# Performance work log

Hardware: AMD Instinct MI355X
Metric: run time of the kernel (lower is better)

## Reference

```python
import jax, jax.numpy as jnp
import numpy as np

NUM_HEADS = 16
HIDDEN = 64  # per-head dim


def setup_inputs() -> dict:
    key = jax.random.key(0)
    ks = jax.random.split(key, 7)
    B, Nq, S, D = 2, 2048, 2048, 1024
    return {
        "queries": jax.random.normal(ks[0], (B, Nq, D), jnp.float32),
        "keys": jax.random.normal(ks[1], (B, S, D), jnp.float32),
        "values": jax.random.normal(ks[2], (B, S, D), jnp.float32),
        "Wq": jax.random.normal(ks[3], (D, NUM_HEADS * HIDDEN), jnp.float32) * 0.02,
        "Wk": jax.random.normal(ks[4], (D, NUM_HEADS * HIDDEN), jnp.float32) * 0.02,
        "Wv": jax.random.normal(ks[5], (D, NUM_HEADS * HIDDEN), jnp.float32) * 0.02,
        "Wo": jax.random.normal(ks[6], (NUM_HEADS * HIDDEN, 1024), jnp.float32) * 0.02,
    }


def reference(queries, keys, values, Wq, Wk, Wv, Wo):
    B, Nq, _ = queries.shape
    S = keys.shape[1]
    H, dh = NUM_HEADS, HIDDEN
    # projections, split heads: [B, len, H, dh] -> [B, H, len, dh]
    Q = (queries @ Wq).reshape(B, Nq, H, dh).transpose(0, 2, 1, 3)
    K = (keys @ Wk).reshape(B, S, H, dh).transpose(0, 2, 1, 3)
    V = (values @ Wv).reshape(B, S, H, dh).transpose(0, 2, 1, 3)
    scores = jnp.einsum("bhqd,bhkd->bhqk", Q, K) / jnp.sqrt(jnp.float32(dh))
    # NOTE: faithful to original -- softmax over ALL keys, THEN multiply by
    # strictly-lower-triangular mask (triangular * (1 - diagonal)); no renorm.
    P = jax.nn.softmax(scores, axis=-1)
    mask = jnp.tril(jnp.ones((Nq, S), jnp.float32), -1)  # strict lower triangle
    Sout = jnp.einsum("bhqk,bhkd->bhqd", P * mask, V)
    merged = Sout.transpose(0, 2, 1, 3).reshape(B, Nq, H * dh)
    return merged @ Wo
```

## Files before the change

kernel.cpp:

```cpp
#include <hip/hip_runtime.h>
#include <hip/hip_bf16.h>
#include <stdint.h>


typedef __bf16 bf16x8 __attribute__((ext_vector_type(8)));
typedef float f32x4 __attribute__((ext_vector_type(4)));

typedef const __attribute__((address_space(1))) void* gas_t;
typedef __attribute__((address_space(3))) void* las_t;

__device__ __forceinline__ unsigned short f2bf(float f) {
    unsigned int u = __float_as_uint(f);
    return (unsigned short)((u + 0x7FFFu + ((u >> 16) & 1u)) >> 16);
}

__global__ __launch_bounds__(256) void cast_qkv(
    const float* __restrict__ q, const float* __restrict__ k, const float* __restrict__ v,
    unsigned short* __restrict__ oq, unsigned short* __restrict__ ok, unsigned short* __restrict__ ov)
{
    const float* src = (blockIdx.z == 0) ? q : (blockIdx.z == 1) ? k : v;
    unsigned short* dst = (blockIdx.z == 0) ? oq : (blockIdx.z == 1) ? ok : ov;
    unsigned int i = blockIdx.x * 256u + threadIdx.x;
    float4 f = reinterpret_cast<const float4*>(src)[i];
    ushort4 o;
    o.x = f2bf(f.x); o.y = f2bf(f.y); o.z = f2bf(f.z); o.w = f2bf(f.w);
    reinterpret_cast<ushort4*>(dst)[i] = o;
}

__global__ __launch_bounds__(256) void transpose_w(
    const float* __restrict__ w0, const float* __restrict__ w1,
    const float* __restrict__ w2, const float* __restrict__ w3,
    unsigned short* __restrict__ t0, unsigned short* __restrict__ t1,
    unsigned short* __restrict__ t2, unsigned short* __restrict__ t3)
{
    const float* W = (blockIdx.z == 0) ? w0 : (blockIdx.z == 1) ? w1 : (blockIdx.z == 2) ? w2 : w3;
    unsigned short* T = (blockIdx.z == 0) ? t0 : (blockIdx.z == 1) ? t1 : (blockIdx.z == 2) ? t2 : t3;
    __shared__ float s[32][33];
    const int tx = threadIdx.x, ty = threadIdx.y;
    const int x = blockIdx.x * 32 + tx;
#pragma unroll
    for (int j = 0; j < 4; ++j)
        s[ty + 8 * j][tx] = W[(size_t)(blockIdx.y * 32 + ty + 8 * j) * 1024 + x];
    __syncthreads();
    const int xo = blockIdx.y * 32 + tx;
#pragma unroll
    for (int j = 0; j < 4; ++j)
        T[(size_t)(blockIdx.x * 32 + ty + 8 * j) * 1024 + xo] = f2bf(s[tx][ty + 8 * j]);
}

__global__ __launch_bounds__(256) void transpose_v(
    const unsigned short* __restrict__ Vp, unsigned short* __restrict__ Vt)
{
    __shared__ unsigned short s[64][68];
    const int tid = threadIdx.x;
    const int s0 = blockIdx.x * 64, h = blockIdx.y, b = blockIdx.z;
    const size_t inbase = ((size_t)(b * 2048 + s0)) * 1024 + h * 64;
#pragma unroll
    for (int r = 0; r < 4; ++r) {
        int idx = r * 256 + tid;
        int row = idx >> 4;
        int c4 = (idx & 15) * 4;
        ushort4 v = *(const ushort4*)(Vp + inbase + (size_t)row * 1024 + c4);
        *(ushort4*)&s[row][c4] = v;
    }
    __syncthreads();
    const size_t outbase = ((size_t)((b * 16 + h) * 64)) * 2048 + s0;
#pragma unroll
    for (int r = 0; r < 4; ++r) {
        int idx = r * 256 + tid;
        int drow = idx >> 4;
        int sc = (idx & 15) * 4;
        ushort4 v;
        v.x = s[sc][drow]; v.y = s[sc + 1][drow]; v.z = s[sc + 2][drow]; v.w = s[sc + 3][drow];
        *(ushort4*)(Vt + outbase + (size_t)drow * 2048 + sc) = v;
    }
}

template <int BM, int BN, int MODE>
__global__ __launch_bounds__(256) void gemm_bt(
    const unsigned short* __restrict__ A0, const unsigned short* __restrict__ A1,
    const unsigned short* __restrict__ A2,
    const unsigned short* __restrict__ B0, const unsigned short* __restrict__ B1,
    const unsigned short* __restrict__ B2,
    unsigned short* __restrict__ C0, unsigned short* __restrict__ C1,
    unsigned short* __restrict__ C2, float* __restrict__ Cf)
{
    constexpr int K = 1024;
    constexpr int WM = BM / 2, WN = BN / 2, MI = WM / 16, NI = WN / 16;
    __shared__ __align__(16) unsigned char lds[(BM + BN) * 64];
    unsigned char* lA = lds;
    unsigned char* lB = lds + BM * 64;

    const int tid = threadIdx.x;
    const int z = blockIdx.z;
    const unsigned short* A  = (MODE == 1 || z == 0) ? A0 : (z == 1) ? A1 : A2;
    const unsigned short* Bt = (MODE == 1 || z == 0) ? B0 : (z == 1) ? B1 : B2;
    const int m0 = blockIdx.y * BM, n0 = blockIdx.x * BN;
    const int w = tid >> 6, lane = tid & 63, g = lane >> 4, l15 = lane & 15;
    const int wr = w >> 1, wc = w & 1;

    f32x4 acc[MI][NI] = {};

    for (int k0 = 0; k0 < K; k0 += 32) {
#pragma unroll
        for (int r = 0; r < (BM * 64) / 4096; ++r) {
            const int o = (r * 256 + tid) * 16;
            const unsigned char* gp = (const unsigned char*)A
                + ((size_t)(m0 + (o >> 6)) * K + k0) * 2 + (o & 63);
            __builtin_amdgcn_global_load_lds((gas_t)gp,
                (las_t)(lA + (r * 256 + (tid & ~63)) * 16), 16, 0, 0);
        }
#pragma unroll
        for (int r = 0; r < (BN * 64) / 4096; ++r) {
            const int o = (r * 256 + tid) * 16;
            const unsigned char* gp = (const unsigned char*)Bt
                + ((size_t)(n0 + (o >> 6)) * K + k0) * 2 + (o & 63);
            __builtin_amdgcn_global_load_lds((gas_t)gp,
                (las_t)(lB + (r * 256 + (tid & ~63)) * 16), 16, 0, 0);
        }
        __syncthreads();

        bf16x8 a[MI], bfr[NI];
#pragma unroll
        for (int mi = 0; mi < MI; ++mi)
            a[mi] = *(const bf16x8*)(lA + (wr * WM + mi * 16 + l15) * 64 + g * 16);
#pragma unroll
        for (int ni = 0; ni < NI; ++ni)
            bfr[ni] = *(const bf16x8*)(lB + (wc * WN + ni * 16 + l15) * 64 + g * 16);
#pragma unroll
        for (int mi = 0; mi < MI; ++mi)
#pragma unroll
            for (int ni = 0; ni < NI; ++ni)
                acc[mi][ni] = __builtin_amdgcn_mfma_f32_16x16x32_bf16(a[mi], bfr[ni], acc[mi][ni], 0, 0, 0);
        __syncthreads();
    }

    if (MODE == 1) {
#pragma unroll
        for (int mi = 0; mi < MI; ++mi)
#pragma unroll
            for (int ni = 0; ni < NI; ++ni)
#pragma unroll
                for (int i = 0; i < 4; ++i) {
                    const int row = m0 + wr * WM + mi * 16 + 4 * g + i;
                    const int col = n0 + wc * WN + ni * 16 + l15;
                    Cf[(size_t)row * 1024 + col] = acc[mi][ni][i];
                }
    } else {
        unsigned short* C = (z == 0) ? C0 : (z == 1) ? C1 : C2;
#pragma unroll
        for (int mi = 0; mi < MI; ++mi)
#pragma unroll
            for (int ni = 0; ni < NI; ++ni)
#pragma unroll
                for (int i = 0; i < 4; ++i) {
                    const int row = m0 + wr * WM + mi * 16 + 4 * g + i;
                    const int col = n0 + wc * WN + ni * 16 + l15;
                    C[(size_t)row * 1024 + col] = f2bf(acc[mi][ni][i]);
                }
    }
}

__device__ __forceinline__ f32x4 qk_exp(const unsigned char* ldsbase, int rowoff,
                                        int ni, int g, int l15,
                                        bf16x8 aq0, bf16x8 aq1)
{
    const int row = rowoff + ni * 16 + l15;
    const int sw = (row & 7) << 4;
    const bf16x8 bk0 = *(const bf16x8*)(ldsbase + ((row * 128 + g * 16) ^ sw));
    const bf16x8 bk1 = *(const bf16x8*)(ldsbase + ((row * 128 + 64 + g * 16) ^ sw));
    f32x4 t = {};
    t = __builtin_amdgcn_mfma_f32_16x16x32_bf16(aq0, bk0, t, 0, 0, 0);
    t = __builtin_amdgcn_mfma_f32_16x16x32_bf16(aq1, bk1, t, 0, 0, 0);
    f32x4 r;
#pragma unroll
    for (int i = 0; i < 4; ++i) r[i] = __expf(t[i] * 0.125f);
    return r;
}

__global__ __launch_bounds__(256) void attn_kernel(
    const unsigned short* __restrict__ Qp, const unsigned short* __restrict__ Kp,
    const unsigned short* __restrict__ Vt, unsigned short* __restrict__ mrg)
{
    __shared__ __align__(16) unsigned char lds[24576];
    unsigned char* Ks = lds;
    unsigned char* Vs = lds + 8192;
    unsigned char* Ps = lds + 16384;

    const int tid = threadIdx.x;
    const int w = tid >> 6, lane = tid & 63, g = lane >> 4, l15 = lane & 15;
    const int bid = blockIdx.x;
    const int bh = (bid & 7) * 4 + ((bid >> 3) & 3);
    const int qt = 31 - (bid >> 5);
    const int b = bh >> 4, h = bh & 15;
    const int q0 = qt * 64;

    bf16x8 aq[2];
    {
        const unsigned short* qp = Qp + ((size_t)(b * 2048 + q0 + 16 * w + l15) * 1024 + h * 64 + g * 8);
        aq[0] = *(const bf16x8*)qp;
        aq[1] = *(const bf16x8*)(qp + 32);
    }

    const unsigned char* Kbase = (const unsigned char*)Kp + ((size_t)(b * 2048) * 1024 + h * 64) * 2;
    const unsigned char* Vbase = (const unsigned char*)Vt + ((size_t)bh * 64) * 2048 * 2;

    f32x4 oacc[4] = {};
    f32x4 dsum = {0.f, 0.f, 0.f, 0.f};

    for (int t = 0; t <= qt; ++t) {
        const int k0 = t * 64;
#pragma unroll
        for (int r = 0; r < 2; ++r) {
            const int o = (r * 256 + tid) * 16;
            const int row = o >> 7;
            const uint4 kv = *(const uint4*)(Kbase + (size_t)(k0 + row) * 2048 + (o & 127));
            *(uint4*)(Ks + (o ^ ((row & 7) << 4))) = kv;
            const uint4 vv = *(const uint4*)(Vbase + (size_t)row * 4096 + (size_t)k0 * 2 + (o & 127));
            *(uint4*)(Vs + (o ^ ((row & 7) << 4))) = vv;
        }
        __syncthreads();

        f32x4 pe[4];
#pragma unroll
        for (int ni = 0; ni < 4; ++ni)
            pe[ni] = qk_exp(Ks, 0, ni, g, l15, aq[0], aq[1]);
        dsum += pe[0] + pe[1] + pe[2] + pe[3];

        if (t == qt) {
#pragma unroll
            for (int ni = 0; ni < 4; ++ni)
#pragma unroll
                for (int i = 0; i < 4; ++i) {
                    const int rloc = 16 * w + 4 * g + i;
                    const int kloc = ni * 16 + l15;
                    const unsigned short pv = (kloc < rloc) ? f2bf(pe[ni][i]) : (unsigned short)0;
                    *(unsigned short*)(Ps + ((rloc * 128 + kloc * 2) ^ ((rloc & 7) << 4))) = pv;
                }
        } else {
#pragma unroll
            for (int ni = 0; ni < 4; ++ni)
#pragma unroll
                for (int i = 0; i < 4; ++i) {
                    const int rloc = 16 * w + 4 * g + i;
                    const int kloc = ni * 16 + l15;
                    *(unsigned short*)(Ps + ((rloc * 128 + kloc * 2) ^ ((rloc & 7) << 4))) = f2bf(pe[ni][i]);
                }
        }

#pragma unroll
        for (int kk = 0; kk < 2; ++kk) {
            const int rowp = 16 * w + l15;
            const bf16x8 pa = *(const bf16x8*)(Ps + ((rowp * 128 + kk * 64 + g * 16) ^ ((rowp & 7) << 4)));
#pragma unroll
            for (int ni = 0; ni < 4; ++ni) {
                const int rv = ni * 16 + l15;
                const bf16x8 bv = *(const bf16x8*)(Vs + ((rv * 128 + kk * 64 + g * 16) ^ ((rv & 7) << 4)));
                oacc[ni] = __builtin_amdgcn_mfma_f32_16x16x32_bf16(pa, bv, oacc[ni], 0, 0, 0);
            }
        }
        __syncthreads();
    }

    for (int k0 = (qt + 1) * 64; k0 < 2048; k0 += 128) {
        const int nk = min(128, 2048 - k0);
        for (int r = 0; r < (nk >> 5); ++r) {
            const int o = (r * 256 + tid) * 16;
            const int row = o >> 7;
            *(uint4*)(lds + (o ^ ((row & 7) << 4))) =
                *(const uint4*)(Kbase + (size_t)(k0 + row) * 2048 + (o & 127));
        }
        __syncthreads();
        for (int koff = 0; koff < nk; koff += 64) {
#pragma unroll
            for (int ni = 0; ni < 4; ++ni) {
                f32x4 pe = qk_exp(lds, koff, ni, g, l15, aq[0], aq[1]);
                dsum += pe;
            }
        }
        __syncthreads();
    }

    float den[4];
#pragma unroll
    for (int i = 0; i < 4; ++i) {
        float rs = dsum[i];
        rs += __shfl_xor(rs, 1, 64);
        rs += __shfl_xor(rs, 2, 64);
        rs += __shfl_xor(rs, 4, 64);
        rs += __shfl_xor(rs, 8, 64);
        den[i] = rs;
    }
#pragma unroll
    for (int ni = 0; ni < 4; ++ni)
#pragma unroll
        for (int i = 0; i < 4; ++i) {
            const int row = q0 + 16 * w + 4 * g + i;
            mrg[((size_t)b * 2048 + row) * 1024 + h * 64 + ni * 16 + l15] =
                f2bf(oacc[ni][i] / den[i]);
        }
}

extern "C" void kernel_launch(void* const* d_in, const int* in_sizes, int n_in,
                              void* d_out, int out_size, void* d_ws, size_t ws_size,
                              hipStream_t stream)
{
    const float* q  = (const float*)d_in[0];
    const float* k  = (const float*)d_in[1];
    const float* v  = (const float*)d_in[2];
    const float* Wq = (const float*)d_in[3];
    const float* Wk = (const float*)d_in[4];
    const float* Wv = (const float*)d_in[5];
    const float* Wo = (const float*)d_in[6];
    float* out = (float*)d_out;

    unsigned short* ws = (unsigned short*)d_ws;
    const size_t TEN = (size_t)2 * 2048 * 1024;
    unsigned short* qbf = ws;
    unsigned short* kbf = ws + TEN;
    unsigned short* vbf = ws + 2 * TEN;
    unsigned short* Wqt = ws + 3 * TEN;
    unsigned short* Wkt = Wqt + 1024 * 1024;
    unsigned short* Wvt = Wkt + 1024 * 1024;
    unsigned short* Wot = Wvt + 1024 * 1024;
    unsigned short* Qp  = ws + 4 * TEN;
    unsigned short* Kp  = ws + 5 * TEN;
    unsigned short* Vp  = ws + 6 * TEN;
    unsigned short* Vt  = qbf;
    unsigned short* mrg = kbf;

    cast_qkv<<<dim3(4096, 1, 3), 256, 0, stream>>>(q, k, v, qbf, kbf, vbf);
    transpose_w<<<dim3(32, 32, 4), dim3(32, 8), 0, stream>>>(Wq, Wk, Wv, Wo, Wqt, Wkt, Wvt, Wot);
    gemm_bt<128, 128, 0><<<dim3(8, 32, 3), 256, 0, stream>>>(
        qbf, kbf, vbf, Wqt, Wkt, Wvt, Qp, Kp, Vp, nullptr);
    transpose_v<<<dim3(32, 16, 2), 256, 0, stream>>>(Vp, Vt);
    attn_kernel<<<dim3(1024, 1, 1), 256, 0, stream>>>(Qp, Kp, Vt, mrg);
    gemm_bt<64, 128, 1><<<dim3(8, 64, 1), 256, 0, stream>>>(
        mrg, nullptr, nullptr, Wot, nullptr, nullptr, nullptr, nullptr, nullptr, out);
}
```

Measured before the change: 232.9 us.

## Prefetch next K/V tiles into registers and transpose QK MFMA for packed P stores

The next K/V tiles (and the first tiles of the denominator-only pass) are now loaded from global memory into registers while the current tile is being computed. This overlaps global memory latency with the MFMA and exp work. The QK MFMA operands are swapped so each lane holds one query row's scores. That lets P be written to LDS as packed bf16 pairs with v_cvt_pk_bf16_f32, and lets the row-sum reduce with two shuffles through a small LDS array. The final division becomes a multiply by a reciprocal. The cost is more live registers, which may reduce occupancy.

```diff
diff --git a/kernel.cpp b/kernel.cpp
--- a/kernel.cpp
+++ b/kernel.cpp
@@ -161,17 +161,17 @@
     }
 }
 
-__device__ __forceinline__ f32x4 qk_exp(const unsigned char* ldsbase, int rowoff,
+__device__ __forceinline__ f32x4 qk_exp(const unsigned char* base, int rowoff,
                                         int ni, int g, int l15,
                                         bf16x8 aq0, bf16x8 aq1)
 {
     const int row = rowoff + ni * 16 + l15;
     const int sw = (row & 7) << 4;
-    const bf16x8 bk0 = *(const bf16x8*)(ldsbase + ((row * 128 + g * 16) ^ sw));
-    const bf16x8 bk1 = *(const bf16x8*)(ldsbase + ((row * 128 + 64 + g * 16) ^ sw));
+    const bf16x8 bk0 = *(const bf16x8*)(base + ((row * 128 + g * 16) ^ sw));
+    const bf16x8 bk1 = *(const bf16x8*)(base + ((row * 128 + 64 + g * 16) ^ sw));
     f32x4 t = {};
-    t = __builtin_amdgcn_mfma_f32_16x16x32_bf16(aq0, bk0, t, 0, 0, 0);
-    t = __builtin_amdgcn_mfma_f32_16x16x32_bf16(aq1, bk1, t, 0, 0, 0);
+    t = __builtin_amdgcn_mfma_f32_16x16x32_bf16(bk0, aq0, t, 0, 0, 0);
+    t = __builtin_amdgcn_mfma_f32_16x16x32_bf16(bk1, aq1, t, 0, 0, 0);
     f32x4 r;
 #pragma unroll
     for (int i = 0; i < 4; ++i) r[i] = __expf(t[i] * 0.125f);
@@ -183,6 +183,7 @@
     const unsigned short* __restrict__ Vt, unsigned short* __restrict__ mrg)
 {
     __shared__ __align__(16) unsigned char lds[24576];
+    __shared__ float dden[4][16];
     unsigned char* Ks = lds;
     unsigned char* Vs = lds + 8192;
     unsigned char* Ps = lds + 16384;
@@ -195,59 +196,81 @@
     const int b = bh >> 4, h = bh & 15;
     const int q0 = qt * 64;
 
-    bf16x8 aq[2];
+    bf16x8 aq0, aq1;
     {
         const unsigned short* qp = Qp + ((size_t)(b * 2048 + q0 + 16 * w + l15) * 1024 + h * 64 + g * 8);
-        aq[0] = *(const bf16x8*)qp;
-        aq[1] = *(const bf16x8*)(qp + 32);
+        aq0 = *(const bf16x8*)qp;
+        aq1 = *(const bf16x8*)(qp + 32);
     }
 
     const unsigned char* Kbase = (const unsigned char*)Kp + ((size_t)(b * 2048) * 1024 + h * 64) * 2;
     const unsigned char* Vbase = (const unsigned char*)Vt + ((size_t)bh * 64) * 2048 * 2;
 
+    const int o0 = tid * 16,         r0 = o0 >> 7;
+    const int o1 = (256 + tid) * 16, r1 = o1 >> 7;
+    const int o2 = (512 + tid) * 16, r2 = o2 >> 7;
+    const int o3 = (768 + tid) * 16, r3 = o3 >> 7;
+
     f32x4 oacc[4] = {};
     f32x4 dsum = {0.f, 0.f, 0.f, 0.f};
 
+    uint4 kr0, kr1, vr0, vr1, cr0, cr1, cr2, cr3;
+    kr0 = *(const uint4*)(Kbase + (size_t)r0 * 2048 + (o0 & 127));
+    kr1 = *(const uint4*)(Kbase + (size_t)r1 * 2048 + (o1 & 127));
+    vr0 = *(const uint4*)(Vbase + (size_t)r0 * 4096 + (o0 & 127));
+    vr1 = *(const uint4*)(Vbase + (size_t)r1 * 4096 + (o1 & 127));
+
     for (int t = 0; t <= qt; ++t) {
-        const int k0 = t * 64;
-#pragma unroll
-        for (int r = 0; r < 2; ++r) {
-            const int o = (r * 256 + tid) * 16;
-            const int row = o >> 7;
-            const uint4 kv = *(const uint4*)(Kbase + (size_t)(k0 + row) * 2048 + (o & 127));
-            *(uint4*)(Ks + (o ^ ((row & 7) << 4))) = kv;
-            const uint4 vv = *(const uint4*)(Vbase + (size_t)row * 4096 + (size_t)k0 * 2 + (o & 127));
-            *(uint4*)(Vs + (o ^ ((row & 7) << 4))) = vv;
+        __syncthreads();
+        *(uint4*)(Ks + (o0 ^ ((r0 & 7) << 4))) = kr0;
+        *(uint4*)(Ks + (o1 ^ ((r1 & 7) << 4))) = kr1;
+        *(uint4*)(Vs + (o0 ^ ((r0 & 7) << 4))) = vr0;
+        *(uint4*)(Vs + (o1 ^ ((r1 & 7) << 4))) = vr1;
+        if (t < qt) {
+            const int k1 = (t + 1) * 64;
+            kr0 = *(const uint4*)(Kbase + (size_t)(k1 + r0) * 2048 + (o0 & 127));
+            kr1 = *(const uint4*)(Kbase + (size_t)(k1 + r1) * 2048 + (o1 & 127));
+            vr0 = *(const uint4*)(Vbase + (size_t)r0 * 4096 + (size_t)k1 * 2 + (o0 & 127));
+            vr1 = *(const uint4*)(Vbase + (size_t)r1 * 4096 + (size_t)k1 * 2 + (o1 & 127));
+        } else if (qt < 31) {
+            const int kc = (qt + 1) * 64;
+            const int nk = 2048 - kc;
+            cr0 = *(const uint4*)(Kbase + (size_t)(kc + r0) * 2048 + (o0 & 127));
+            cr1 = *(const uint4*)(Kbase + (size_t)(kc + r1) * 2048 + (o1 & 127));
+            if (nk > 64) {
+                cr2 = *(const uint4*)(Kbase + (size_t)(kc + r2) * 2048 + (o2 & 127));
+                cr3 = *(const uint4*)(Kbase + (size_t)(kc + r3) * 2048 + (o3 & 127));
+            }
         }
         __syncthreads();
 
         f32x4 pe[4];
 #pragma unroll
-        for (int ni = 0; ni < 4; ++ni)
-            pe[ni] = qk_exp(Ks, 0, ni, g, l15, aq[0], aq[1]);
-        dsum += pe[0] + pe[1] + pe[2] + pe[3];
-
+        for (int ni = 0; ni < 4; ++ni) {
+            pe[ni] = qk_exp(Ks, 0, ni, g, l15, aq0, aq1);
+            dsum += pe[ni];
+        }
         if (t == qt) {
+            const int qloc = 16 * w + l15;
 #pragma unroll
             for (int ni = 0; ni < 4; ++ni)
 #pragma unroll
-                for (int i = 0; i < 4; ++i) {
-                    const int rloc = 16 * w + 4 * g + i;
-                    const int kloc = ni * 16 + l15;
-                    const unsigned short pv = (kloc < rloc) ? f2bf(pe[ni][i]) : (unsigned short)0;
-                    *(unsigned short*)(Ps + ((rloc * 128 + kloc * 2) ^ ((rloc & 7) << 4))) = pv;
-                }
-        } else {
-#pragma unroll
-            for (int ni = 0; ni < 4; ++ni)
-#pragma unroll
-                for (int i = 0; i < 4; ++i) {
-                    const int rloc = 16 * w + 4 * g + i;
-                    const int kloc = ni * 16 + l15;
-                    *(unsigned short*)(Ps + ((rloc * 128 + kloc * 2) ^ ((rloc & 7) << 4))) = f2bf(pe[ni][i]);
-                }
-        }
-
+                for (int i = 0; i < 4; ++i)
+                    if (ni * 16 + 4 * g + i >= qloc) pe[ni][i] = 0.f;
+        }
+        {
+            const int prow = 16 * w + l15;
+            const int pbase = prow * 128;
+            const int sw = (prow & 7) << 4;
+#pragma unroll
+            for (int ni = 0; ni < 4; ++ni) {
+                unsigned int lo, hi;
+                asm("v_cvt_pk_bf16_f32 %0, %1, %2" : "=v"(lo) : "v"(pe[ni][0]), "v"(pe[ni][1]));
+                asm("v_cvt_pk_bf16_f32 %0, %1, %2" : "=v"(hi) : "v"(pe[ni][2]), "v"(pe[ni][3]));
+                uint2 pv; pv.x = lo; pv.y = hi;
+                *(uint2*)(Ps + ((pbase + ni * 32 + g * 8) ^ sw)) = pv;
+            }
+        }
 #pragma unroll
         for (int kk = 0; kk < 2; ++kk) {
             const int rowp = 16 * w + l15;
@@ -259,45 +282,48 @@
                 oacc[ni] = __builtin_amdgcn_mfma_f32_16x16x32_bf16(pa, bv, oacc[ni], 0, 0, 0);
             }
         }
-        __syncthreads();
-    }
-
-    for (int k0 = (qt + 1) * 64; k0 < 2048; k0 += 128) {
-        const int nk = min(128, 2048 - k0);
-        for (int r = 0; r < (nk >> 5); ++r) {
-            const int o = (r * 256 + tid) * 16;
-            const int row = o >> 7;
-            *(uint4*)(lds + (o ^ ((row & 7) << 4))) =
-                *(const uint4*)(Kbase + (size_t)(k0 + row) * 2048 + (o & 127));
-        }
-        __syncthreads();
-        for (int koff = 0; koff < nk; koff += 64) {
-#pragma unroll
-            for (int ni = 0; ni < 4; ++ni) {
-                f32x4 pe = qk_exp(lds, koff, ni, g, l15, aq[0], aq[1]);
-                dsum += pe;
+    }
+
+    for (int kc = (qt + 1) * 64; kc < 2048; kc += 128) {
+        const int nk = min(128, 2048 - kc);
+        __syncthreads();
+        *(uint4*)(lds + (o0 ^ ((r0 & 7) << 4))) = cr0;
+        *(uint4*)(lds + (o1 ^ ((r1 & 7) << 4))) = cr1;
+        if (nk > 64) {
+            *(uint4*)(lds + (o2 ^ ((r2 & 7) << 4))) = cr2;
+            *(uint4*)(lds + (o3 ^ ((r3 & 7) << 4))) = cr3;
+        }
+        const int kn = kc + 128;
+        if (kn < 2048) {
+            const int nk2 = 2048 - kn;
+            cr0 = *(const uint4*)(Kbase + (size_t)(kn + r0) * 2048 + (o0 & 127));
+            cr1 = *(const uint4*)(Kbase + (size_t)(kn + r1) * 2048 + (o1 & 127));
+            if (nk2 > 64) {
+                cr2 = *(const uint4*)(Kbase + (size_t)(kn + r2) * 2048 + (o2 & 127));
+                cr3 = *(const uint4*)(Kbase + (size_t)(kn + r3) * 2048 + (o3 & 127));
             }
         }
         __syncthreads();
-    }
-
-    float den[4];
-#pragma unroll
-    for (int i = 0; i < 4; ++i) {
-        float rs = dsum[i];
-        rs += __shfl_xor(rs, 1, 64);
-        rs += __shfl_xor(rs, 2, 64);
-        rs += __shfl_xor(rs, 4, 64);
-        rs += __shfl_xor(rs, 8, 64);
-        den[i] = rs;
-    }
+        for (int koff = 0; koff < nk; koff += 64)
+#pragma unroll
+            for (int ni = 0; ni < 4; ++ni)
+                dsum += qk_exp(lds, koff, ni, g, l15, aq0, aq1);
+    }
+
+    float den = dsum[0] + dsum[1] + dsum[2] + dsum[3];
+    den += __shfl_xor(den, 16, 64);
+    den += __shfl_xor(den, 32, 64);
+    if (lane < 16) dden[w][lane] = den;
+    float inv[4];
+#pragma unroll
+    for (int i = 0; i < 4; ++i) inv[i] = 1.0f / dden[w][4 * g + i];
 #pragma unroll
     for (int ni = 0; ni < 4; ++ni)
 #pragma unroll
         for (int i = 0; i < 4; ++i) {
             const int row = q0 + 16 * w + 4 * g + i;
             mrg[((size_t)b * 2048 + row) * 1024 + h * 64 + ni * 16 + l15] =
-                f2bf(oacc[ni][i] / den[i]);
+                f2bf(oacc[ni][i] * inv[i]);
         }
 }
 
```

Result: no change. 234.2 us (+0.6%).
